# Kernel optimization log

Hardware: AMD Instinct MI355X
Metric: run time of the kernel (lower is better)

## Reference

```python
import jax, jax.numpy as jnp
import numpy as np
from jax import lax

B, H, OUT, STEPS = 256, 512, 9, 325  # 1 initial step + 325 unrolled steps = 326 outputs


def setup_inputs() -> dict:
    key = jax.random.key(0)
    ks = jax.random.split(key, 12)
    s = 0.05
    return {
        "x": jax.random.normal(ks[0], (B, H), jnp.float32),
        "hx0": jax.random.normal(ks[1], (B, H), jnp.float32),
        "cx0": jax.random.normal(ks[2], (B, H), jnp.float32),
        "W_ih": jax.random.normal(ks[3], (4 * H, H), jnp.float32) * s,
        "W_hh": jax.random.normal(ks[4], (4 * H, H), jnp.float32) * s,
        "b_ih": jax.random.normal(ks[5], (4 * H,), jnp.float32) * s,
        "b_hh": jax.random.normal(ks[6], (4 * H,), jnp.float32) * s,
        "W1": jax.random.normal(ks[7], (H, H), jnp.float32) * s,
        "b1": jax.random.normal(ks[8], (H,), jnp.float32) * s,
        "W2": jax.random.normal(ks[9], (OUT, H), jnp.float32) * s,
        "b2": jax.random.normal(ks[10], (OUT,), jnp.float32) * s,
    }


def reference(x, hx0, cx0, W_ih, W_hh, b_ih, b_hh, W1, b1, W2, b2):
    def lstm_cell(inp, h, c):
        # PyTorch LSTMCell gate order: i, f, g, o
        gates = inp @ W_ih.T + b_ih + h @ W_hh.T + b_hh  # [B, 4H]
        i, f, g, o = jnp.split(gates, 4, axis=-1)
        i = jax.nn.sigmoid(i)
        f = jax.nn.sigmoid(f)
        g = jnp.tanh(g)
        o = jax.nn.sigmoid(o)
        c_new = f * c + i * g
        h_new = o * jnp.tanh(c_new)
        return h_new, c_new

    def mlp(h):
        return jax.nn.relu(h @ W1.T + b1) @ W2.T + b2  # [B, 9]

    h, c = lstm_cell(x, hx0, cx0)
    y0 = mlp(h)

    def step(carry, _):
        h, c = carry
        # original: self.cell(hx, (hx, cx)) -- input IS the current hidden state
        h, c = lstm_cell(h, h, c)
        return (h, c), mlp(h)

    _, ys = lax.scan(step, (h, c), None, length=STEPS)  # ys: [325, B, 9]
    out = jnp.concatenate([y0[None], ys], axis=0)  # [326, B, 9]
    return jnp.transpose(out, (1, 0, 2))  # [B, 326, 9]
```

## Files before the change

kernel.cpp:

```cpp
#include <hip/hip_runtime.h>
#include <cstdio>

#define B_   256
#define H_   512
#define G4_  2048
#define T_   326
#define OUT_ 9

typedef __attribute__((ext_vector_type(8))) short s16x8;
typedef __attribute__((ext_vector_type(4))) float f32x4;
typedef unsigned long long ull;

__device__ inline unsigned short to_bf16(float f) {
    unsigned int u = __builtin_bit_cast(unsigned int, f);
    unsigned int r = (u + 0x7fffu + ((u >> 16) & 1u)) >> 16;
    return (unsigned short)r;
}

__device__ inline float sigmoidf_(float x) { return 1.0f / (1.0f + __expf(-x)); }

__device__ inline float fast_tanh(float x) {
    x = fminf(fmaxf(x, -15.f), 15.f);
    float e = __expf(2.f * x);
    return (e - 1.f) / (e + 1.f);
}


__global__ void prep_weights(const float* __restrict__ Wih, const float* __restrict__ Whh,
                             const float* __restrict__ bih, const float* __restrict__ bhh,
                             unsigned short* __restrict__ Wc, unsigned short* __restrict__ Wcat,
                             float* __restrict__ bc) {
    int idx = blockIdx.x * 256 + threadIdx.x;
    int n = idx >> 9, k = idx & 511;
    float wi = Wih[idx], wh = Whh[idx];
    Wc[idx] = to_bf16(wi + wh);
    Wcat[(n << 10) + k]       = to_bf16(wi);
    Wcat[(n << 10) + 512 + k] = to_bf16(wh);
    if (k == 0) bc[n] = bih[n] + bhh[n];
}

__global__ void prep_w1(const float* __restrict__ W1, unsigned short* __restrict__ W1b) {
    int idx = blockIdx.x * 256 + threadIdx.x;
    W1b[idx] = to_bf16(W1[idx]);
}

__global__ void prep_w2(const float* __restrict__ W2, unsigned short* __restrict__ W2b) {
    int idx = blockIdx.x * 256 + threadIdx.x;
    int o = idx >> 9, k = idx & 511;
    W2b[idx] = (o < OUT_) ? to_bf16(W2[o * H_ + k]) : (unsigned short)0;
}

__global__ void prep_x(const float* __restrict__ x, const float* __restrict__ hx0,
                       unsigned short* __restrict__ xcat) {
    int idx = blockIdx.x * 256 + threadIdx.x;
    int b = idx >> 9, k = idx & 511;
    xcat[(b << 10) + k]       = to_bf16(x[idx]);
    xcat[(b << 10) + 512 + k] = to_bf16(hx0[idx]);
}

template <int KLEN>
__global__ __launch_bounds__(256) void lstm_step(
    const unsigned short* __restrict__ A,
    const unsigned short* __restrict__ W,
    const float* __restrict__ bc,
    const float* __restrict__ c_in,
    float* __restrict__ c_out,
    unsigned short* __restrict__ h_out) {
    const int lane = threadIdx.x & 63;
    const int wave = threadIdx.x >> 6;
    const int mn = lane & 15, q = lane >> 4;
    const int rt = blockIdx.x & 15;
    const int hb = (blockIdx.x >> 4) * 64 + wave * 16;

    const unsigned short* ap  = A + (size_t)(rt * 16 + mn) * KLEN + q * 8;
    const unsigned short* wp0 = W + (size_t)(0 * H_ + hb + mn) * KLEN + q * 8;
    const unsigned short* wp1 = W + (size_t)(1 * H_ + hb + mn) * KLEN + q * 8;
    const unsigned short* wp2 = W + (size_t)(2 * H_ + hb + mn) * KLEN + q * 8;
    const unsigned short* wp3 = W + (size_t)(3 * H_ + hb + mn) * KLEN + q * 8;

    f32x4 acc0 = {0.f,0.f,0.f,0.f}, acc1 = {0.f,0.f,0.f,0.f};
    f32x4 acc2 = {0.f,0.f,0.f,0.f}, acc3 = {0.f,0.f,0.f,0.f};
#pragma unroll 4
    for (int k0 = 0; k0 < KLEN; k0 += 32) {
        s16x8 a  = *reinterpret_cast<const s16x8*>(ap + k0);
        s16x8 w0 = *reinterpret_cast<const s16x8*>(wp0 + k0);
        s16x8 w1 = *reinterpret_cast<const s16x8*>(wp1 + k0);
        s16x8 w2 = *reinterpret_cast<const s16x8*>(wp2 + k0);
        s16x8 w3 = *reinterpret_cast<const s16x8*>(wp3 + k0);
        acc0 = __builtin_amdgcn_mfma_f32_16x16x32_bf16(a, w0, acc0, 0, 0, 0);
        acc1 = __builtin_amdgcn_mfma_f32_16x16x32_bf16(a, w1, acc1, 0, 0, 0);
        acc2 = __builtin_amdgcn_mfma_f32_16x16x32_bf16(a, w2, acc2, 0, 0, 0);
        acc3 = __builtin_amdgcn_mfma_f32_16x16x32_bf16(a, w3, acc3, 0, 0, 0);
    }

    const int j = hb + mn;
    const float bi = bc[j], bfv = bc[H_ + j], bg = bc[2 * H_ + j], bo = bc[3 * H_ + j];
#pragma unroll
    for (int r = 0; r < 4; ++r) {
        const int row = rt * 16 + q * 4 + r;
        const float iv = sigmoidf_(acc0[r] + bi);
        const float fv = sigmoidf_(acc1[r] + bfv);
        const float gv = fast_tanh(acc2[r] + bg);
        const float ov = sigmoidf_(acc3[r] + bo);
        const float co = c_in[row * H_ + j];
        const float cn = fv * co + iv * gv;
        c_out[row * H_ + j] = cn;
        h_out[row * H_ + j] = to_bf16(ov * fast_tanh(cn));
    }
}

__global__ __launch_bounds__(256) void lstm_persist(
    const unsigned short* __restrict__ Wc,
    const float* __restrict__ bc,
    const float* __restrict__ c0,
    unsigned short* __restrict__ h_hist,
    unsigned int* __restrict__ ctr,
    const unsigned short* __restrict__ W1b,
    const float* __restrict__ b1,
    const unsigned short* __restrict__ W2b,
    const float* __restrict__ b2,
    float* __restrict__ ws_y) {
    __shared__ unsigned short A_lds[16 * 512];
    __shared__ float gate_lds[4 * 16 * 33];
    __shared__ unsigned short z_lds[2 * 16 * 24];
    const int tid = threadIdx.x;
    const int lane = tid & 63, wave = tid >> 6;
    const int mn = lane & 15, q = lane >> 4;
    const int g  = blockIdx.x & 15;
    const int wg = blockIdx.x >> 4;
    const int jb = wg * 32;
    unsigned int* ctr_g = ctr + g * 32;

    s16x8 breg[2][16];
#pragma unroll
    for (int n = 0; n < 2; ++n) {
        const unsigned short* wp = Wc + (size_t)(wave * H_ + jb + n * 16 + mn) * H_ + q * 8;
#pragma unroll
        for (int kk = 0; kk < 16; ++kk)
            breg[n][kk] = *reinterpret_cast<const s16x8*>(wp + kk * 32);
    }
    const float bcv0 = bc[wave * H_ + jb + mn];
    const float bcv1 = bc[wave * H_ + jb + 16 + mn];

    const int crow = tid >> 4, cc0 = (tid & 15) * 2;
    float c_x = c0[(size_t)(g * 16 + crow) * H_ + jb + cc0];
    float c_y = c0[(size_t)(g * 16 + crow) * H_ + jb + cc0 + 1];

    int a_st[8];
#pragma unroll
    for (int p = 0; p < 8; ++p) {
        const int qi = p * 256 + tid;
        const int row = qi >> 7;
        const int bcol = (qi & 127) * 8;
        a_st[p] = row * 512 + ((bcol ^ ((row & 7) << 4)) >> 1);
    }
    int a_rd[16];
#pragma unroll
    for (int kk = 0; kk < 16; ++kk) {
        const int bcol = kk * 64 + q * 16;
        a_rd[kk] = mn * 512 + ((bcol ^ ((mn & 7) << 4)) >> 1);
    }

    s16x8 w1reg[16];
    s16x8 w2reg = {0,0,0,0,0,0,0,0};
    float b1v = 0.f, b2v = 0.f;
    const int zw = wave - 2;
    if (wave >= 2) {
        const int zbase = wg * 32 + zw * 16;
        const unsigned short* wp = W1b + (size_t)(zbase + mn) * H_ + q * 8;
#pragma unroll
        for (int kk = 0; kk < 16; ++kk)
            w1reg[kk] = *reinterpret_cast<const s16x8*>(wp + kk * 32);
        b1v = b1[zbase + mn];
        if (q < 2)
            w2reg = *reinterpret_cast<const s16x8*>(W2b + (size_t)mn * H_ + zbase + q * 8);
        b2v = (mn < OUT_ && wg == 0 && wave == 2) ? b2[mn] : 0.f;
    }

    auto mlp_pass = [&](int tout) {
        f32x4 zacc = {0.f,0.f,0.f,0.f};
#pragma unroll
        for (int kk = 0; kk < 16; ++kk) {
            s16x8 a = *reinterpret_cast<const s16x8*>(&A_lds[a_rd[kk]]);
            zacc = __builtin_amdgcn_mfma_f32_16x16x32_bf16(a, w1reg[kk], zacc, 0, 0, 0);
        }
#pragma unroll
        for (int r = 0; r < 4; ++r) {
            float v = zacc[r] + b1v;
            v = v > 0.f ? v : 0.f;
            z_lds[zw * 384 + (q * 4 + r) * 24 + mn] = to_bf16(v);
        }
        s16x8 az = {0,0,0,0,0,0,0,0};
        if (q < 2) az = *reinterpret_cast<const s16x8*>(&z_lds[zw * 384 + mn * 24 + q * 8]);
        f32x4 y = __builtin_amdgcn_mfma_f32_16x16x32_bf16(az, w2reg, f32x4{0.f,0.f,0.f,0.f}, 0, 0, 0);
        if (mn < OUT_) {
#pragma unroll
            for (int r = 0; r < 4; ++r)
                atomicAdd(&ws_y[(size_t)(g * 16 + q * 4 + r) * (T_ * OUT_) + tout * OUT_ + mn],
                          y[r] + b2v);
        }
    };

    for (int t = 1; t < T_; ++t) {
        const ull* hsrc64 = reinterpret_cast<const ull*>(
            h_hist + (size_t)(t - 1) * (B_ * H_) + (size_t)g * 16 * H_);
        ull vv[8];
#pragma unroll
        for (int p = 0; p < 8; ++p)
            vv[p] = __hip_atomic_load(hsrc64 + p * 256 + tid, __ATOMIC_RELAXED,
                                      __HIP_MEMORY_SCOPE_AGENT);
#pragma unroll
        for (int p = 0; p < 8; ++p)
            *reinterpret_cast<ull*>(&A_lds[a_st[p]]) = vv[p];
        __syncthreads();

        f32x4 acc0 = {0.f,0.f,0.f,0.f}, acc1 = {0.f,0.f,0.f,0.f};
#pragma unroll
        for (int kk = 0; kk < 16; ++kk) {
            s16x8 a = *reinterpret_cast<const s16x8*>(&A_lds[a_rd[kk]]);
            acc0 = __builtin_amdgcn_mfma_f32_16x16x32_bf16(a, breg[0][kk], acc0, 0, 0, 0);
            acc1 = __builtin_amdgcn_mfma_f32_16x16x32_bf16(a, breg[1][kk], acc1, 0, 0, 0);
        }

#pragma unroll
        for (int r = 0; r < 4; ++r) {
            float v0 = acc0[r] + bcv0, v1 = acc1[r] + bcv1;
            if (wave == 2) { v0 = fast_tanh(v0); v1 = fast_tanh(v1); }
            else           { v0 = sigmoidf_(v0); v1 = sigmoidf_(v1); }
            gate_lds[(wave * 16 + (q * 4 + r)) * 33 + mn]      = v0;
            gate_lds[(wave * 16 + (q * 4 + r)) * 33 + 16 + mn] = v1;
        }
        __syncthreads();

        {
            float iv0 = gate_lds[(0 * 16 + crow) * 33 + cc0], iv1 = gate_lds[(0 * 16 + crow) * 33 + cc0 + 1];
            float fv0 = gate_lds[(1 * 16 + crow) * 33 + cc0], fv1 = gate_lds[(1 * 16 + crow) * 33 + cc0 + 1];
            float gv0 = gate_lds[(2 * 16 + crow) * 33 + cc0], gv1 = gate_lds[(2 * 16 + crow) * 33 + cc0 + 1];
            float ov0 = gate_lds[(3 * 16 + crow) * 33 + cc0], ov1 = gate_lds[(3 * 16 + crow) * 33 + cc0 + 1];
            c_x = fv0 * c_x + iv0 * gv0;
            c_y = fv1 * c_y + iv1 * gv1;
            unsigned int h0 = to_bf16(ov0 * fast_tanh(c_x));
            unsigned int h1 = to_bf16(ov1 * fast_tanh(c_y));
            unsigned int packed = h0 | (h1 << 16);
            unsigned int* hdst = reinterpret_cast<unsigned int*>(
                h_hist + (size_t)t * (B_ * H_) + (size_t)(g * 16 + crow) * H_ + jb + cc0);
            __hip_atomic_store(hdst, packed, __ATOMIC_RELAXED, __HIP_MEMORY_SCOPE_AGENT);
        }

        __syncthreads();
        asm volatile("" ::: "memory");
        if (tid == 0) {
            __hip_atomic_fetch_add(ctr_g, 1u, __ATOMIC_RELAXED, __HIP_MEMORY_SCOPE_AGENT);
            const unsigned int target = 16u * (unsigned int)t;
            while (__hip_atomic_load(ctr_g, __ATOMIC_RELAXED, __HIP_MEMORY_SCOPE_AGENT) < target) {
            }
        }
        if (wave >= 2) mlp_pass(t - 1);
        asm volatile("" ::: "memory");
        __syncthreads();
    }

    {
        const ull* hsrc64 = reinterpret_cast<const ull*>(
            h_hist + (size_t)(T_ - 1) * (B_ * H_) + (size_t)g * 16 * H_);
        ull vv[8];
#pragma unroll
        for (int p = 0; p < 8; ++p)
            vv[p] = __hip_atomic_load(hsrc64 + p * 256 + tid, __ATOMIC_RELAXED,
                                      __HIP_MEMORY_SCOPE_AGENT);
#pragma unroll
        for (int p = 0; p < 8; ++p)
            *reinterpret_cast<ull*>(&A_lds[a_st[p]]) = vv[p];
        __syncthreads();
        if (wave >= 2) mlp_pass(T_ - 1);
    }
}

__global__ void copy_out(const float* __restrict__ ws_y, float* __restrict__ out) {
    int idx = blockIdx.x * 256 + threadIdx.x;
    out[idx] = ws_y[idx];
}

extern "C" void kernel_launch(void* const* d_in, const int* in_sizes, int n_in,
                              void* d_out, int out_size, void* d_ws, size_t ws_size,
                              hipStream_t stream) {
    (void)in_sizes; (void)n_in; (void)out_size;
    const float* x   = (const float*)d_in[0];
    const float* hx0 = (const float*)d_in[1];
    const float* cx0 = (const float*)d_in[2];
    const float* Wih = (const float*)d_in[3];
    const float* Whh = (const float*)d_in[4];
    const float* bih = (const float*)d_in[5];
    const float* bhh = (const float*)d_in[6];
    const float* W1  = (const float*)d_in[7];
    const float* b1  = (const float*)d_in[8];
    const float* W2  = (const float*)d_in[9];
    const float* b2  = (const float*)d_in[10];
    float* out = (float*)d_out;

    char* p = (char*)d_ws;
    size_t off = 0;
    auto alloc = [&](size_t bytes) {
        void* r = p + off;
        off = (off + bytes + 255) & ~(size_t)255;
        return r;
    };
    unsigned short* Wc     = (unsigned short*)alloc((size_t)G4_ * H_ * 2);
    unsigned short* Wcat   = (unsigned short*)alloc((size_t)G4_ * 1024 * 2);
    unsigned short* W1b    = (unsigned short*)alloc((size_t)H_ * H_ * 2);
    unsigned short* W2b    = (unsigned short*)alloc((size_t)16 * H_ * 2);
    float*          bc     = (float*)alloc((size_t)G4_ * 4);
    unsigned short* xcat   = (unsigned short*)alloc((size_t)B_ * 1024 * 2);
    float*          cbuf   = (float*)alloc((size_t)B_ * H_ * 4);
    unsigned int*   ctr    = (unsigned int*)alloc(4096);
    float*          ws_y   = (float*)alloc((size_t)B_ * T_ * OUT_ * 4);
    unsigned short* h_hist = (unsigned short*)alloc((size_t)T_ * B_ * H_ * 2);
    if (off > ws_size) {
        fprintf(stderr, "kernel_launch: ws too small: need %zu have %zu\n", off, ws_size);
        return;
    }

    prep_weights<<<G4_ * H_ / 256, 256, 0, stream>>>(Wih, Whh, bih, bhh, Wc, Wcat, bc);
    prep_w1<<<H_ * H_ / 256, 256, 0, stream>>>(W1, W1b);
    prep_w2<<<16 * H_ / 256, 256, 0, stream>>>(W2, W2b);
    prep_x<<<B_ * H_ / 256, 256, 0, stream>>>(x, hx0, xcat);

    lstm_step<1024><<<128, 256, 0, stream>>>(xcat, Wcat, bc, cx0, cbuf, h_hist);

    hipMemsetAsync(ctr, 0, 4096, stream);
    hipMemsetAsync(ws_y, 0, (size_t)B_ * T_ * OUT_ * 4, stream);

    lstm_persist<<<256, 256, 0, stream>>>(Wc, bc, cbuf, h_hist, ctr,
                                          W1b, b1, W2b, b2, ws_y);

    copy_out<<<(B_ * T_ * OUT_) / 256, 256, 0, stream>>>(ws_y, out);
}
```

Measured before the change: 1.045 ms.

## Move MLP head to dedicated consumer blocks overlapping the LSTM recurrence

```diff
diff --git a/kernel.cpp b/kernel.cpp
--- a/kernel.cpp
+++ b/kernel.cpp
@@ -119,32 +119,14 @@
     const float* __restrict__ b1,
     const unsigned short* __restrict__ W2b,
     const float* __restrict__ b2,
-    float* __restrict__ ws_y) {
-    __shared__ unsigned short A_lds[16 * 512];
-    __shared__ float gate_lds[4 * 16 * 33];
-    __shared__ unsigned short z_lds[2 * 16 * 24];
+    float* __restrict__ out) {
+    __shared__ ull smem[4128];
+    unsigned short* A_lds = reinterpret_cast<unsigned short*>(smem);
+    float* gate_lds = reinterpret_cast<float*>(reinterpret_cast<char*>(smem) + 16384);
+    unsigned short* z_lds = reinterpret_cast<unsigned short*>(reinterpret_cast<char*>(smem) + 16384);
     const int tid = threadIdx.x;
     const int lane = tid & 63, wave = tid >> 6;
     const int mn = lane & 15, q = lane >> 4;
-    const int g  = blockIdx.x & 15;
-    const int wg = blockIdx.x >> 4;
-    const int jb = wg * 32;
-    unsigned int* ctr_g = ctr + g * 32;
-
-    s16x8 breg[2][16];
-#pragma unroll
-    for (int n = 0; n < 2; ++n) {
-        const unsigned short* wp = Wc + (size_t)(wave * H_ + jb + n * 16 + mn) * H_ + q * 8;
-#pragma unroll
-        for (int kk = 0; kk < 16; ++kk)
-            breg[n][kk] = *reinterpret_cast<const s16x8*>(wp + kk * 32);
-    }
-    const float bcv0 = bc[wave * H_ + jb + mn];
-    const float bcv1 = bc[wave * H_ + jb + 16 + mn];
-
-    const int crow = tid >> 4, cc0 = (tid & 15) * 2;
-    float c_x = c0[(size_t)(g * 16 + crow) * H_ + jb + cc0];
-    float c_y = c0[(size_t)(g * 16 + crow) * H_ + jb + cc0 + 1];
 
     int a_st[8];
 #pragma unroll
@@ -161,124 +143,158 @@
         a_rd[kk] = mn * 512 + ((bcol ^ ((mn & 7) << 4)) >> 1);
     }
 
-    s16x8 w1reg[16];
-    s16x8 w2reg = {0,0,0,0,0,0,0,0};
-    float b1v = 0.f, b2v = 0.f;
-    const int zw = wave - 2;
-    if (wave >= 2) {
-        const int zbase = wg * 32 + zw * 16;
-        const unsigned short* wp = W1b + (size_t)(zbase + mn) * H_ + q * 8;
-#pragma unroll
-        for (int kk = 0; kk < 16; ++kk)
-            w1reg[kk] = *reinterpret_cast<const s16x8*>(wp + kk * 32);
-        b1v = b1[zbase + mn];
-        if (q < 2)
-            w2reg = *reinterpret_cast<const s16x8*>(W2b + (size_t)mn * H_ + zbase + q * 8);
-        b2v = (mn < OUT_ && wg == 0 && wave == 2) ? b2[mn] : 0.f;
-    }
-
-    auto mlp_pass = [&](int tout) {
-        f32x4 zacc = {0.f,0.f,0.f,0.f};
-#pragma unroll
-        for (int kk = 0; kk < 16; ++kk) {
-            s16x8 a = *reinterpret_cast<const s16x8*>(&A_lds[a_rd[kk]]);
-            zacc = __builtin_amdgcn_mfma_f32_16x16x32_bf16(a, w1reg[kk], zacc, 0, 0, 0);
+    if (blockIdx.x < 256) {
+        const int g  = blockIdx.x & 15;
+        const int jb = (blockIdx.x >> 4) * 32;
+        unsigned int* ctr_g = ctr + g * 32;
+
+        s16x8 breg[2][16];
+#pragma unroll
+        for (int n = 0; n < 2; ++n) {
+            const unsigned short* wp = Wc + (size_t)(wave * H_ + jb + n * 16 + mn) * H_ + q * 8;
+#pragma unroll
+            for (int kk = 0; kk < 16; ++kk)
+                breg[n][kk] = *reinterpret_cast<const s16x8*>(wp + kk * 32);
         }
-#pragma unroll
-        for (int r = 0; r < 4; ++r) {
-            float v = zacc[r] + b1v;
-            v = v > 0.f ? v : 0.f;
-            z_lds[zw * 384 + (q * 4 + r) * 24 + mn] = to_bf16(v);
+        const float bcv0 = bc[wave * H_ + jb + mn];
+        const float bcv1 = bc[wave * H_ + jb + 16 + mn];
+
+        const int crow = tid >> 4, cc0 = (tid & 15) * 2;
+        float c_x = c0[(size_t)(g * 16 + crow) * H_ + jb + cc0];
+        float c_y = c0[(size_t)(g * 16 + crow) * H_ + jb + cc0 + 1];
+
+        for (int t = 1; t < T_; ++t) {
+            const ull* hsrc64 = reinterpret_cast<const ull*>(
+                h_hist + (size_t)(t - 1) * (B_ * H_) + (size_t)g * 16 * H_);
+            ull vv[8];
+#pragma unroll
+            for (int p = 0; p < 8; ++p)
+                vv[p] = __hip_atomic_load(hsrc64 + p * 256 + tid, __ATOMIC_RELAXED,
+                                          __HIP_MEMORY_SCOPE_AGENT);
+#pragma unroll
+            for (int p = 0; p < 8; ++p)
+                *reinterpret_cast<ull*>(&A_lds[a_st[p]]) = vv[p];
+            __syncthreads();
+
+            f32x4 acc0 = {0.f,0.f,0.f,0.f}, acc1 = {0.f,0.f,0.f,0.f};
+#pragma unroll
+            for (int kk = 0; kk < 16; ++kk) {
+                s16x8 a = *reinterpret_cast<const s16x8*>(&A_lds[a_rd[kk]]);
+                acc0 = __builtin_amdgcn_mfma_f32_16x16x32_bf16(a, breg[0][kk], acc0, 0, 0, 0);
+                acc1 = __builtin_amdgcn_mfma_f32_16x16x32_bf16(a, breg[1][kk], acc1, 0, 0, 0);
+            }
+
+#pragma unroll
+            for (int r = 0; r < 4; ++r) {
+                float v0 = acc0[r] + bcv0, v1 = acc1[r] + bcv1;
+                if (wave == 2) { v0 = fast_tanh(v0); v1 = fast_tanh(v1); }
+                else           { v0 = sigmoidf_(v0); v1 = sigmoidf_(v1); }
+                gate_lds[(wave * 16 + (q * 4 + r)) * 33 + mn]      = v0;
+                gate_lds[(wave * 16 + (q * 4 + r)) * 33 + 16 + mn] = v1;
+            }
+            __syncthreads();
+
+            {
+                float iv0 = gate_lds[(0 * 16 + crow) * 33 + cc0], iv1 = gate_lds[(0 * 16 + crow) * 33 + cc0 + 1];
+                float fv0 = gate_lds[(1 * 16 + crow) * 33 + cc0], fv1 = gate_lds[(1 * 16 + crow) * 33 + cc0 + 1];
+                float gv0 = gate_lds[(2 * 16 + crow) * 33 + cc0], gv1 = gate_lds[(2 * 16 + crow) * 33 + cc0 + 1];
+                float ov0 = gate_lds[(3 * 16 + crow) * 33 + cc0], ov1 = gate_lds[(3 * 16 + crow) * 33 + cc0 + 1];
+                c_x = fv0 * c_x + iv0 * gv0;
+                c_y = fv1 * c_y + iv1 * gv1;
+                unsigned int h0 = to_bf16(ov0 * fast_tanh(c_x));
+                unsigned int h1 = to_bf16(ov1 * fast_tanh(c_y));
+                unsigned int packed = h0 | (h1 << 16);
+                unsigned int* hdst = reinterpret_cast<unsigned int*>(
+                    h_hist + (size_t)t * (B_ * H_) + (size_t)(g * 16 + crow) * H_ + jb + cc0);
+                __hip_atomic_store(hdst, packed, __ATOMIC_RELAXED, __HIP_MEMORY_SCOPE_AGENT);
+            }
+
+            __syncthreads();
+            asm volatile("" ::: "memory");
+            if (tid == 0) {
+                __hip_atomic_fetch_add(ctr_g, 1u, __ATOMIC_RELAXED, __HIP_MEMORY_SCOPE_AGENT);
+                if (t < T_ - 1) {
+                    const unsigned int target = 16u * (unsigned int)t;
+                    while (__hip_atomic_load(ctr_g, __ATOMIC_RELAXED,
+                                             __HIP_MEMORY_SCOPE_AGENT) < target) {
+                    }
+                }
+            }
+            asm volatile("" ::: "memory");
+            if (t < T_ - 1) __syncthreads();
         }
-        s16x8 az = {0,0,0,0,0,0,0,0};
-        if (q < 2) az = *reinterpret_cast<const s16x8*>(&z_lds[zw * 384 + mn * 24 + q * 8]);
-        f32x4 y = __builtin_amdgcn_mfma_f32_16x16x32_bf16(az, w2reg, f32x4{0.f,0.f,0.f,0.f}, 0, 0, 0);
-        if (mn < OUT_) {
-#pragma unroll
-            for (int r = 0; r < 4; ++r)
-                atomicAdd(&ws_y[(size_t)(g * 16 + q * 4 + r) * (T_ * OUT_) + tout * OUT_ + mn],
-                          y[r] + b2v);
+    } else {
+        const int j = blockIdx.x - 256;
+        const int xcd = j & 7, mid = j >> 3;
+
+        float b1v[8];
+#pragma unroll
+        for (int nt = 0; nt < 8; ++nt) b1v[nt] = b1[wave * 128 + nt * 16 + mn];
+        const float b2v = (mn < OUT_) ? b2[mn] : 0.f;
+
+        for (int i = mid; i < 2 * T_; i += 16) {
+            const int t = i >> 1;
+            const int g = xcd + 8 * (i & 1);
+
+            if (tid == 0) {
+                const unsigned int tgt = 16u * (unsigned int)t;
+                while (__hip_atomic_load(ctr + g * 32, __ATOMIC_RELAXED,
+                                         __HIP_MEMORY_SCOPE_AGENT) < tgt)
+                    __builtin_amdgcn_s_sleep(4);
+            }
+            __syncthreads();
+
+            const ull* hsrc64 = reinterpret_cast<const ull*>(
+                h_hist + (size_t)t * (B_ * H_) + (size_t)g * 16 * H_);
+            ull vv[8];
+#pragma unroll
+            for (int p = 0; p < 8; ++p)
+                vv[p] = __hip_atomic_load(hsrc64 + p * 256 + tid, __ATOMIC_RELAXED,
+                                          __HIP_MEMORY_SCOPE_AGENT);
+#pragma unroll
+            for (int p = 0; p < 8; ++p)
+                *reinterpret_cast<ull*>(&A_lds[a_st[p]]) = vv[p];
+            __syncthreads();
+
+            f32x4 acc[8];
+#pragma unroll
+            for (int nt = 0; nt < 8; ++nt) acc[nt] = f32x4{0.f,0.f,0.f,0.f};
+            for (int kk = 0; kk < 16; ++kk) {
+                s16x8 a = *reinterpret_cast<const s16x8*>(&A_lds[a_rd[kk]]);
+#pragma unroll
+                for (int nt = 0; nt < 8; ++nt) {
+                    s16x8 b = *reinterpret_cast<const s16x8*>(
+                        W1b + (size_t)(wave * 128 + nt * 16 + mn) * H_ + kk * 32 + q * 8);
+                    acc[nt] = __builtin_amdgcn_mfma_f32_16x16x32_bf16(a, b, acc[nt], 0, 0, 0);
+                }
+            }
+#pragma unroll
+            for (int nt = 0; nt < 8; ++nt)
+#pragma unroll
+                for (int r = 0; r < 4; ++r) {
+                    float v = acc[nt][r] + b1v[nt];
+                    v = v > 0.f ? v : 0.f;
+                    z_lds[(q * 4 + r) * 520 + wave * 128 + nt * 16 + mn] = to_bf16(v);
+                }
+            __syncthreads();
+
+            if (wave == 0) {
+                f32x4 y = {0.f,0.f,0.f,0.f};
+#pragma unroll 4
+                for (int k0 = 0; k0 < 512; k0 += 32) {
+                    s16x8 az = *reinterpret_cast<const s16x8*>(&z_lds[mn * 520 + k0 + q * 8]);
+                    s16x8 bw = *reinterpret_cast<const s16x8*>(W2b + (size_t)mn * H_ + k0 + q * 8);
+                    y = __builtin_amdgcn_mfma_f32_16x16x32_bf16(az, bw, y, 0, 0, 0);
+                }
+                if (mn < OUT_) {
+#pragma unroll
+                    for (int r = 0; r < 4; ++r)
+                        out[(size_t)(g * 16 + q * 4 + r) * (T_ * OUT_) + t * OUT_ + mn] = y[r] + b2v;
+                }
+            }
+            __syncthreads();
         }
-    };
-
-    for (int t = 1; t < T_; ++t) {
-        const ull* hsrc64 = reinterpret_cast<const ull*>(
-            h_hist + (size_t)(t - 1) * (B_ * H_) + (size_t)g * 16 * H_);
-        ull vv[8];
-#pragma unroll
-        for (int p = 0; p < 8; ++p)
-            vv[p] = __hip_atomic_load(hsrc64 + p * 256 + tid, __ATOMIC_RELAXED,
-                                      __HIP_MEMORY_SCOPE_AGENT);
-#pragma unroll
-        for (int p = 0; p < 8; ++p)
-            *reinterpret_cast<ull*>(&A_lds[a_st[p]]) = vv[p];
-        __syncthreads();
-
-        f32x4 acc0 = {0.f,0.f,0.f,0.f}, acc1 = {0.f,0.f,0.f,0.f};
-#pragma unroll
-        for (int kk = 0; kk < 16; ++kk) {
-            s16x8 a = *reinterpret_cast<const s16x8*>(&A_lds[a_rd[kk]]);
-            acc0 = __builtin_amdgcn_mfma_f32_16x16x32_bf16(a, breg[0][kk], acc0, 0, 0, 0);
-            acc1 = __builtin_amdgcn_mfma_f32_16x16x32_bf16(a, breg[1][kk], acc1, 0, 0, 0);
-        }
-
-#pragma unroll
-        for (int r = 0; r < 4; ++r) {
-            float v0 = acc0[r] + bcv0, v1 = acc1[r] + bcv1;
-            if (wave == 2) { v0 = fast_tanh(v0); v1 = fast_tanh(v1); }
-            else           { v0 = sigmoidf_(v0); v1 = sigmoidf_(v1); }
-            gate_lds[(wave * 16 + (q * 4 + r)) * 33 + mn]      = v0;
-            gate_lds[(wave * 16 + (q * 4 + r)) * 33 + 16 + mn] = v1;
-        }
-        __syncthreads();
-
-        {
-            float iv0 = gate_lds[(0 * 16 + crow) * 33 + cc0], iv1 = gate_lds[(0 * 16 + crow) * 33 + cc0 + 1];
-            float fv0 = gate_lds[(1 * 16 + crow) * 33 + cc0], fv1 = gate_lds[(1 * 16 + crow) * 33 + cc0 + 1];
-            float gv0 = gate_lds[(2 * 16 + crow) * 33 + cc0], gv1 = gate_lds[(2 * 16 + crow) * 33 + cc0 + 1];
-            float ov0 = gate_lds[(3 * 16 + crow) * 33 + cc0], ov1 = gate_lds[(3 * 16 + crow) * 33 + cc0 + 1];
-            c_x = fv0 * c_x + iv0 * gv0;
-            c_y = fv1 * c_y + iv1 * gv1;
-            unsigned int h0 = to_bf16(ov0 * fast_tanh(c_x));
-            unsigned int h1 = to_bf16(ov1 * fast_tanh(c_y));
-            unsigned int packed = h0 | (h1 << 16);
-            unsigned int* hdst = reinterpret_cast<unsigned int*>(
-                h_hist + (size_t)t * (B_ * H_) + (size_t)(g * 16 + crow) * H_ + jb + cc0);
-            __hip_atomic_store(hdst, packed, __ATOMIC_RELAXED, __HIP_MEMORY_SCOPE_AGENT);
-        }
-
-        __syncthreads();
-        asm volatile("" ::: "memory");
-        if (tid == 0) {
-            __hip_atomic_fetch_add(ctr_g, 1u, __ATOMIC_RELAXED, __HIP_MEMORY_SCOPE_AGENT);
-            const unsigned int target = 16u * (unsigned int)t;
-            while (__hip_atomic_load(ctr_g, __ATOMIC_RELAXED, __HIP_MEMORY_SCOPE_AGENT) < target) {
-            }
-        }
-        if (wave >= 2) mlp_pass(t - 1);
-        asm volatile("" ::: "memory");
-        __syncthreads();
-    }
-
-    {
-        const ull* hsrc64 = reinterpret_cast<const ull*>(
-            h_hist + (size_t)(T_ - 1) * (B_ * H_) + (size_t)g * 16 * H_);
-        ull vv[8];
-#pragma unroll
-        for (int p = 0; p < 8; ++p)
-            vv[p] = __hip_atomic_load(hsrc64 + p * 256 + tid, __ATOMIC_RELAXED,
-                                      __HIP_MEMORY_SCOPE_AGENT);
-#pragma unroll
-        for (int p = 0; p < 8; ++p)
-            *reinterpret_cast<ull*>(&A_lds[a_st[p]]) = vv[p];
-        __syncthreads();
-        if (wave >= 2) mlp_pass(T_ - 1);
-    }
-}
-
-__global__ void copy_out(const float* __restrict__ ws_y, float* __restrict__ out) {
-    int idx = blockIdx.x * 256 + threadIdx.x;
-    out[idx] = ws_y[idx];
+    }
 }
 
 extern "C" void kernel_launch(void* const* d_in, const int* in_sizes, int n_in,
@@ -313,7 +329,6 @@
     unsigned short* xcat   = (unsigned short*)alloc((size_t)B_ * 1024 * 2);
     float*          cbuf   = (float*)alloc((size_t)B_ * H_ * 4);
     unsigned int*   ctr    = (unsigned int*)alloc(4096);
-    float*          ws_y   = (float*)alloc((size_t)B_ * T_ * OUT_ * 4);
     unsigned short* h_hist = (unsigned short*)alloc((size_t)T_ * B_ * H_ * 2);
     if (off > ws_size) {
         fprintf(stderr, "kernel_launch: ws too small: need %zu have %zu\n", off, ws_size);
@@ -328,10 +343,6 @@
     lstm_step<1024><<<128, 256, 0, stream>>>(xcat, Wcat, bc, cx0, cbuf, h_hist);
 
     hipMemsetAsync(ctr, 0, 4096, stream);
-    hipMemsetAsync(ws_y, 0, (size_t)B_ * T_ * OUT_ * 4, stream);
-
-    lstm_persist<<<256, 256, 0, stream>>>(Wc, bc, cbuf, h_hist, ctr,
-                                          W1b, b1, W2b, b2, ws_y);
-
-    copy_out<<<(B_ * T_ * OUT_) / 256, 256, 0, stream>>>(ws_y, out);
-}
+    lstm_persist<<<384, 256, 0, stream>>>(Wc, bc, cbuf, h_hist, ctr,
+                                          W1b, b1, W2b, b2, out);
+}
```

After: 1.178 ms. +12.7%, slower.
